# Kernel tuning notes

Hardware: AMD Instinct MI355X
Metric: run time of the kernel (lower is better)

## Reference

```python
import jax, jax.numpy as jnp
import numpy as np

N_EVENTS = 131072
N_FEATURES = 128
N_GLOBAL = 64
HIDDEN = 512
N_BRANCHES = 2


def setup_inputs() -> dict:
    key = jax.random.key(0)
    ks = jax.random.split(key, 4)
    x = jax.random.normal(ks[0], (N_EVENTS, N_FEATURES), dtype=jnp.float32)
    global_features = jax.random.normal(ks[1], (N_EVENTS, N_GLOBAL), dtype=jnp.float32)
    # proj_nn params: Linear(192->512) + LeakyReLU + Linear(512->256)
    W1 = jax.random.normal(ks[2], (N_FEATURES + N_GLOBAL, HIDDEN), dtype=jnp.float32) / np.sqrt(N_FEATURES + N_GLOBAL)
    b1 = jnp.zeros((HIDDEN,), dtype=jnp.float32)
    W2 = jax.random.normal(ks[3], (HIDDEN, N_BRANCHES * N_FEATURES), dtype=jnp.float32) / np.sqrt(HIDDEN)
    b2 = jnp.zeros((N_BRANCHES * N_FEATURES,), dtype=jnp.float32)
    # isplit=0: root node idxs = arange(n_events)
    parents_idxs = jnp.arange(N_EVENTS, dtype=jnp.int64 if jax.config.jax_enable_x64 else jnp.int32)
    return {"x": x, "global_features": global_features, "W1": W1, "b1": b1,
            "W2": W2, "b2": b2, "parents_idxs": parents_idxs}


def reference(x, global_features, W1, b1, W2, b2, parents_idxs):
    n_events, n_features = x.shape
    n_branches = N_BRANCHES
    n_parents = parents_idxs.shape[0] // n_events  # = 1 at isplit=0
    # gather parent node features and per-event global features
    parent_global = global_features[parents_idxs % n_events, :]   # [P*E, G]
    parents_ftxs = x[parents_idxs, :]                             # [P*E, F]
    # proj_nn: Linear -> LeakyReLU -> Linear
    h = jnp.concatenate([parents_ftxs, parent_global], axis=1)
    h = jax.nn.leaky_relu(h @ W1 + b1)                            # slope 0.01, torch default
    proj_ftx = h @ W2 + b2                                        # [P*E, B*F]
    # reshape_features: out[p, b, e] = proj[e + p*E, b*F:(b+1)*F]
    children_ftxs = (proj_ftx
                     .reshape(n_parents, n_events, n_branches, n_features)
                     .transpose(0, 2, 1, 3)
                     .reshape(n_parents * n_branches * n_events, n_features))
    return jnp.concatenate([x, children_ftxs], axis=0)
```

## Files before the change

kernel.cpp:

```cpp
#include <hip/hip_runtime.h>
#include <hip/hip_bf16.h>

#define NEV 131072
#define NF 128
#define NG 64
#define KIN 192
#define NH 512
#define NOUT 256
#define BM 128
#define NT 512
#define NBLK (NEV / BM)
#define LDS128 131072

typedef __bf16 bf16x8 __attribute__((ext_vector_type(8)));
typedef __bf16 bf16x4 __attribute__((ext_vector_type(4)));
typedef float f32x4 __attribute__((ext_vector_type(4)));

__device__ __forceinline__ int a_off(int r, int cb) { return r * 384 + (cb ^ ((r & 7) << 4)); }
__device__ __forceinline__ int h_off(int r, int cb) { return r * 1024 + (cb ^ ((r & 7) << 4)); }

__global__ void pack_w(const float* __restrict__ W1, const float* __restrict__ W2,
                       __bf16* __restrict__ w1p, __bf16* __restrict__ w2p) {
    int t = blockIdx.x * blockDim.x + threadIdx.x;
    if (t < KIN * NH) {
        int j = t & 7;
        int lane = (t >> 3) & 63;
        int n = (t >> 9) & 3;
        int r = t >> 11;
        int kk = r % 6;
        int wc = r / 6;
        int lg = lane >> 4, lr = lane & 15;
        int k = kk * 32 + lg * 8 + j;
        int col = wc * 64 + n * 16 + lr;
        w1p[t] = (__bf16)W1[(size_t)k * NH + col];
    } else {
        int u = t - KIN * NH;
        if (u < NH * NOUT) {
            int j = u & 7;
            int lane = (u >> 3) & 63;
            int n = (u >> 9) & 1;
            int r = u >> 10;
            int kk = r & 15;
            int wc = r >> 4;
            int lg = lane >> 4, lr = lane & 15;
            int k = kk * 32 + lg * 8 + j;
            int col = wc * 32 + n * 16 + lr;
            w2p[u] = (__bf16)W2[(size_t)k * NOUT + col];
        }
    }
}

__global__ __launch_bounds__(NT)
__attribute__((amdgpu_waves_per_eu(2, 2))) void fused128(
        const float* __restrict__ x, const float* __restrict__ gf,
        const __bf16* __restrict__ w1p, const float* __restrict__ b1,
        const __bf16* __restrict__ w2p, const float* __restrict__ b2,
        const int* __restrict__ idx, float* __restrict__ out) {
    extern __shared__ __align__(16) unsigned char smem[];

    const int tid = threadIdx.x;
    const int wc = tid >> 6;
    const int lane = tid & 63;
    const int lg = lane >> 4;
    const int lr = lane & 15;
    const int row0 = blockIdx.x * BM;

    bf16x8 bcur[4];
    {
        const __bf16* wp = w1p;
        asm volatile("" : "+s"(wp));
#pragma unroll
        for (int n = 0; n < 4; ++n)
            bcur[n] = *(const bf16x8*)(wp + (size_t)((wc * 6 + 0) * 4 + n) * 512 + lane * 8);
    }

    const f32x4* x4 = (const f32x4*)x;
    const f32x4* g4 = (const f32x4*)gf;
    f32x4* o4 = (f32x4*)out;
#pragma unroll
    for (int q = tid; q < BM * (NF / 4); q += NT) {
        int r = q >> 5, c4 = q & 31;
        int e = row0 + r;
        int p = idx[e];
        f32x4 v = x4[(size_t)e * 32 + c4];
        __builtin_nontemporal_store(v, &o4[(size_t)e * 32 + c4]);
        f32x4 vs = v;
        if (p != e) vs = x4[(size_t)p * 32 + c4];
        bf16x4 tb = {(__bf16)vs[0], (__bf16)vs[1], (__bf16)vs[2], (__bf16)vs[3]};
        *(bf16x4*)(smem + a_off(r, c4 * 8)) = tb;
    }
#pragma unroll
    for (int q = tid; q < BM * (NG / 4); q += NT) {
        int r = q >> 4, c4 = q & 15;
        int e = row0 + r;
        int p = idx[e] & (NEV - 1);
        f32x4 vs = g4[(size_t)p * 16 + c4];
        bf16x4 tb = {(__bf16)vs[0], (__bf16)vs[1], (__bf16)vs[2], (__bf16)vs[3]};
        *(bf16x4*)(smem + a_off(r, 256 + c4 * 8)) = tb;
    }
    __syncthreads();

    f32x4 acc1T[4][8] = {};
#pragma unroll
    for (int kk = 0; kk < KIN / 32; ++kk) {
        bf16x8 bnxt[4];
        if (kk + 1 < KIN / 32) {
            const __bf16* wp = w1p;
            asm volatile("" : "+s"(wp));
#pragma unroll
            for (int n = 0; n < 4; ++n)
                bnxt[n] = *(const bf16x8*)(wp + (size_t)((wc * 6 + kk + 1) * 4 + n) * 512 + lane * 8);
        }
        int kbyte = kk * 64 + lg * 16;
        bf16x8 a[8];
#pragma unroll
        for (int m = 0; m < 8; ++m)
            a[m] = *(const bf16x8*)(smem + a_off(m * 16 + lr, kbyte));
        __builtin_amdgcn_s_setprio(1);
#pragma unroll
        for (int n = 0; n < 4; ++n)
#pragma unroll
            for (int m = 0; m < 8; ++m)
                acc1T[n][m] = __builtin_amdgcn_mfma_f32_16x16x32_bf16(bcur[n], a[m], acc1T[n][m], 0, 0, 0);
        __builtin_amdgcn_s_setprio(0);
        if (kk + 1 < KIN / 32) {
#pragma unroll
            for (int n = 0; n < 4; ++n) bcur[n] = bnxt[n];
        }
        __builtin_amdgcn_sched_barrier(0);
    }

    bf16x8 ccur[2];
    {
        const __bf16* wp = w2p;
        asm volatile("" : "+s"(wp));
#pragma unroll
        for (int n = 0; n < 2; ++n)
            ccur[n] = *(const bf16x8*)(wp + (size_t)((wc * 16 + 0) * 2 + n) * 512 + lane * 8);
    }
    __syncthreads();

#pragma unroll
    for (int n = 0; n < 4; ++n) {
        int c0 = wc * 64 + n * 16 + lg * 4;
        f32x4 bb = *(const f32x4*)(b1 + c0);
#pragma unroll
        for (int m = 0; m < 8; ++m) {
            int e = m * 16 + lr;
            bf16x4 tb;
#pragma unroll
            for (int i = 0; i < 4; ++i) {
                float v = acc1T[n][m][i] + bb[i];
                v = (v >= 0.f) ? v : 0.01f * v;
                tb[i] = (__bf16)v;
            }
            *(bf16x4*)(smem + h_off(e, c0 * 2)) = tb;
        }
    }
    __syncthreads();

    f32x4 acc2T[2][8] = {};
#pragma unroll
    for (int kk = 0; kk < NH / 32; ++kk) {
        bf16x8 cnxt[2];
        if (kk + 1 < NH / 32) {
            const __bf16* wp = w2p;
            asm volatile("" : "+s"(wp));
#pragma unroll
            for (int n = 0; n < 2; ++n)
                cnxt[n] = *(const bf16x8*)(wp + (size_t)((wc * 16 + kk + 1) * 2 + n) * 512 + lane * 8);
        }
        int kbyte = kk * 64 + lg * 16;
        bf16x8 a2[8];
#pragma unroll
        for (int m = 0; m < 8; ++m)
            a2[m] = *(const bf16x8*)(smem + h_off(m * 16 + lr, kbyte));
        __builtin_amdgcn_s_setprio(1);
#pragma unroll
        for (int n = 0; n < 2; ++n)
#pragma unroll
            for (int m = 0; m < 8; ++m)
                acc2T[n][m] = __builtin_amdgcn_mfma_f32_16x16x32_bf16(ccur[n], a2[m], acc2T[n][m], 0, 0, 0);
        __builtin_amdgcn_s_setprio(0);
        if (kk + 1 < NH / 32) {
#pragma unroll
            for (int n = 0; n < 2; ++n) ccur[n] = cnxt[n];
        }
        __builtin_amdgcn_sched_barrier(0);
    }

    float* ob = out + ((size_t)NEV * (1 + (wc >> 2))) * NF;
#pragma unroll
    for (int m = 0; m < 8; ++m) {
        size_t ebase = (size_t)(row0 + m * 16 + lr) * NF;
#pragma unroll
        for (int n = 0; n < 2; ++n) {
            int col = wc * 32 + n * 16 + lg * 4;
            f32x4 bb = *(const f32x4*)(b2 + col);
            f32x4 v = acc2T[n][m] + bb;
            __builtin_nontemporal_store(v, (f32x4*)(ob + ebase + (col & 127)));
        }
    }
}

template <bool TW>
__global__ __launch_bounds__(512, 2) void fused_mlp(
        const float* __restrict__ x, const float* __restrict__ gf,
        const __bf16* __restrict__ w1p, const float* __restrict__ W1f,
        const float* __restrict__ b1,
        const __bf16* __restrict__ w2p, const float* __restrict__ W2f,
        const float* __restrict__ b2,
        const int* __restrict__ idx,
        float* __restrict__ out) {
    __shared__ __align__(16) unsigned char smem[65536];

    const int tid = threadIdx.x;
    const int wid = tid >> 6;
    const int lane = tid & 63;
    const int lg = lane >> 4;
    const int lr = lane & 15;
    const int row0 = blockIdx.x * 64;

    bf16x8 b1r[KIN / 32][4];
#pragma unroll
    for (int kk = 0; kk < KIN / 32; ++kk)
#pragma unroll
        for (int n = 0; n < 4; ++n) {
            if (TW) {
                b1r[kk][n] = *(const bf16x8*)(w1p + (size_t)(((wid * 6 + kk) * 4 + n) * 64 + lane) * 8);
            } else {
                int col = wid * 64 + n * 16 + lr;
                const float* wcp = W1f + (size_t)(kk * 32 + lg * 8) * NH + col;
#pragma unroll
                for (int i = 0; i < 8; ++i) b1r[kk][n][i] = (__bf16)wcp[(size_t)i * NH];
            }
        }

    const f32x4* x4 = (const f32x4*)x;
    const f32x4* g4 = (const f32x4*)gf;
    f32x4* o4 = (f32x4*)out;
    for (int q = tid; q < 64 * (NF / 4); q += 512) {
        int r = q >> 5, c4 = q & 31;
        int e = row0 + r;
        int p = idx[e];
        f32x4 v = x4[(size_t)e * 32 + c4];
        __builtin_nontemporal_store(v, &o4[(size_t)e * 32 + c4]);
        f32x4 vs = v;
        if (p != e) vs = x4[(size_t)p * 32 + c4];
        bf16x4 tb = {(__bf16)vs[0], (__bf16)vs[1], (__bf16)vs[2], (__bf16)vs[3]};
        *(bf16x4*)(smem + a_off(r, c4 * 8)) = tb;
    }
    for (int q = tid; q < 64 * (NG / 4); q += 512) {
        int r = q >> 4, c4 = q & 15;
        int e = row0 + r;
        int p = idx[e] & (NEV - 1);
        f32x4 vs = g4[(size_t)p * 16 + c4];
        bf16x4 tb = {(__bf16)vs[0], (__bf16)vs[1], (__bf16)vs[2], (__bf16)vs[3]};
        *(bf16x4*)(smem + a_off(r, 256 + c4 * 8)) = tb;
    }
    __syncthreads();

    f32x4 acc1T[4][4] = {};
#pragma unroll
    for (int kk = 0; kk < KIN / 32; ++kk) {
        int kbyte = kk * 64 + lg * 16;
        bf16x8 a[4];
#pragma unroll
        for (int m = 0; m < 4; ++m)
            a[m] = *(const bf16x8*)(smem + a_off(m * 16 + lr, kbyte));
        __builtin_amdgcn_s_setprio(1);
#pragma unroll
        for (int n = 0; n < 4; ++n)
#pragma unroll
            for (int m = 0; m < 4; ++m)
                acc1T[n][m] = __builtin_amdgcn_mfma_f32_16x16x32_bf16(b1r[kk][n], a[m], acc1T[n][m], 0, 0, 0);
        __builtin_amdgcn_s_setprio(0);
    }

    bf16x8 b2r[NH / 32][2];
#pragma unroll
    for (int kk = 0; kk < NH / 32; ++kk)
#pragma unroll
        for (int n = 0; n < 2; ++n) {
            if (TW) {
                b2r[kk][n] = *(const bf16x8*)(w2p + (size_t)(((wid * 16 + kk) * 2 + n) * 64 + lane) * 8);
            } else {
                int col = wid * 32 + n * 16 + lr;
                const float* wcp = W2f + (size_t)(kk * 32 + lg * 8) * NOUT + col;
#pragma unroll
                for (int i = 0; i < 8; ++i) b2r[kk][n][i] = (__bf16)wcp[(size_t)i * NOUT];
            }
        }

    __syncthreads();

#pragma unroll
    for (int n = 0; n < 4; ++n) {
        f32x4 bb = *(const f32x4*)(b1 + wid * 64 + n * 16 + lg * 4);
        int cb = (wid * 64 + n * 16 + lg * 4) * 2;
#pragma unroll
        for (int m = 0; m < 4; ++m) {
            int e = m * 16 + lr;
            bf16x4 tb;
#pragma unroll
            for (int i = 0; i < 4; ++i) {
                float v = acc1T[n][m][i] + bb[i];
                v = (v >= 0.f) ? v : 0.01f * v;
                tb[i] = (__bf16)v;
            }
            *(bf16x4*)(smem + h_off(e, cb)) = tb;
        }
    }
    __syncthreads();

    f32x4 acc2T[2][4] = {};
#pragma unroll
    for (int kk = 0; kk < NH / 32; ++kk) {
        int kbyte = kk * 64 + lg * 16;
        bf16x8 a2[4];
#pragma unroll
        for (int m = 0; m < 4; ++m)
            a2[m] = *(const bf16x8*)(smem + h_off(m * 16 + lr, kbyte));
        __builtin_amdgcn_s_setprio(1);
#pragma unroll
        for (int n = 0; n < 2; ++n)
#pragma unroll
            for (int m = 0; m < 4; ++m)
                acc2T[n][m] = __builtin_amdgcn_mfma_f32_16x16x32_bf16(b2r[kk][n], a2[m], acc2T[n][m], 0, 0, 0);
        __builtin_amdgcn_s_setprio(0);
    }

    float* ob = out + ((size_t)NEV * (1 + (wid >> 2))) * NF;
#pragma unroll
    for (int m = 0; m < 4; ++m) {
        size_t ebase = (size_t)(row0 + m * 16 + lr) * NF;
#pragma unroll
        for (int n = 0; n < 2; ++n) {
            int col = wid * 32 + n * 16 + lg * 4;
            f32x4 bb = *(const f32x4*)(b2 + col);
            f32x4 v = acc2T[n][m] + bb;
            __builtin_nontemporal_store(v, (f32x4*)(ob + ebase + (col & 127)));
        }
    }
}

extern "C" void kernel_launch(void* const* d_in, const int* in_sizes, int n_in,
                              void* d_out, int out_size, void* d_ws, size_t ws_size,
                              hipStream_t stream) {
    const float* x  = (const float*)d_in[0];
    const float* gf = (const float*)d_in[1];
    const float* W1 = (const float*)d_in[2];
    const float* b1 = (const float*)d_in[3];
    const float* W2 = (const float*)d_in[4];
    const float* b2 = (const float*)d_in[5];
    const int*  idx = (const int*)d_in[6];
    float* out = (float*)d_out;

    const size_t wbytes = (size_t)(KIN * NH + NH * NOUT) * sizeof(__bf16);
    int tot = KIN * NH + NH * NOUT;

    if (ws_size >= wbytes) {
        __bf16* w1p = (__bf16*)d_ws;
        __bf16* w2p = w1p + KIN * NH;
        pack_w<<<(tot + 511) / 512, 512, 0, stream>>>(W1, W2, w1p, w2p);
        hipError_t st = hipFuncSetAttribute(
            (const void*)fused128, hipFuncAttributeMaxDynamicSharedMemorySize, LDS128);
        if (st == hipSuccess) {
            fused128<<<NBLK, NT, LDS128, stream>>>(x, gf, w1p, b1, w2p, b2, idx, out);
        } else {
            fused_mlp<true><<<NEV / 64, 512, 0, stream>>>(x, gf, w1p, nullptr, b1,
                                                          w2p, nullptr, b2, idx, out);
        }
    } else {
        fused_mlp<false><<<NEV / 64, 512, 0, stream>>>(x, gf, nullptr, W1, b1,
                                                       nullptr, W2, b2, idx, out);
    }
}
```

Measured before the change: 102.2 us.

## Make fused MLP kernel loop over tiles with double-buffered input staging

```diff
diff --git a/kernel.cpp b/kernel.cpp
--- a/kernel.cpp
+++ b/kernel.cpp
@@ -7,10 +7,13 @@
 #define KIN 192
 #define NH 512
 #define NOUT 256
-#define BM 128
+#define BM 64
 #define NT 512
-#define NBLK (NEV / BM)
-#define LDS128 131072
+#define TILES 8
+#define NPERS (NEV / (BM * TILES))
+#define ABYTES 24576
+#define HBASE (2 * ABYTES)
+#define LDSTOT (HBASE + BM * NH * 2)
 
 typedef __bf16 bf16x8 __attribute__((ext_vector_type(8)));
 typedef __bf16 bf16x4 __attribute__((ext_vector_type(4)));
@@ -51,7 +54,7 @@
 }
 
 __global__ __launch_bounds__(NT)
-__attribute__((amdgpu_waves_per_eu(2, 2))) void fused128(
+__attribute__((amdgpu_waves_per_eu(2, 2))) void fused_pers(
         const float* __restrict__ x, const float* __restrict__ gf,
         const __bf16* __restrict__ w1p, const float* __restrict__ b1,
         const __bf16* __restrict__ w2p, const float* __restrict__ b2,
@@ -63,8 +66,51 @@
     const int lane = tid & 63;
     const int lg = lane >> 4;
     const int lr = lane & 15;
-    const int row0 = blockIdx.x * BM;
-
+
+    const f32x4* x4 = (const f32x4*)x;
+    const f32x4* g4 = (const f32x4*)gf;
+    f32x4* o4 = (f32x4*)out;
+    const int xr = tid >> 5, xc = tid & 31;
+    const int gr = tid >> 4, gc = tid & 15;
+
+    f32x4 xv[4], xs[4], gv[2];
+
+    auto stage_issue = [&](int row0) {
+#pragma unroll
+        for (int s = 0; s < 4; ++s) {
+            int e = row0 + xr + 16 * s;
+            int p = idx[e];
+            xv[s] = x4[(size_t)e * 32 + xc];
+            xs[s] = xv[s];
+            if (p != e) xs[s] = x4[(size_t)p * 32 + xc];
+        }
+#pragma unroll
+        for (int s = 0; s < 2; ++s) {
+            int e = row0 + gr + 32 * s;
+            int p = idx[e] & (NEV - 1);
+            gv[s] = g4[(size_t)p * 16 + gc];
+        }
+    };
+    auto stage_commit = [&](int row0, int ab) {
+#pragma unroll
+        for (int s = 0; s < 4; ++s) {
+            int r = xr + 16 * s;
+            __builtin_nontemporal_store(xv[s], &o4[(size_t)(row0 + r) * 32 + xc]);
+            bf16x4 tb = {(__bf16)xs[s][0], (__bf16)xs[s][1], (__bf16)xs[s][2], (__bf16)xs[s][3]};
+            *(bf16x4*)(smem + ab + a_off(r, xc * 8)) = tb;
+        }
+#pragma unroll
+        for (int s = 0; s < 2; ++s) {
+            int r = gr + 32 * s;
+            bf16x4 tb = {(__bf16)gv[s][0], (__bf16)gv[s][1], (__bf16)gv[s][2], (__bf16)gv[s][3]};
+            *(bf16x4*)(smem + ab + a_off(r, 256 + gc * 8)) = tb;
+        }
+    };
+
+    int row0 = blockIdx.x * (BM * TILES);
+
+    stage_issue(row0);
+    stage_commit(row0, 0);
     bf16x8 bcur[4];
     {
         const __bf16* wp = w1p;
@@ -73,133 +119,126 @@
         for (int n = 0; n < 4; ++n)
             bcur[n] = *(const bf16x8*)(wp + (size_t)((wc * 6 + 0) * 4 + n) * 512 + lane * 8);
     }
-
-    const f32x4* x4 = (const f32x4*)x;
-    const f32x4* g4 = (const f32x4*)gf;
-    f32x4* o4 = (f32x4*)out;
-#pragma unroll
-    for (int q = tid; q < BM * (NF / 4); q += NT) {
-        int r = q >> 5, c4 = q & 31;
-        int e = row0 + r;
-        int p = idx[e];
-        f32x4 v = x4[(size_t)e * 32 + c4];
-        __builtin_nontemporal_store(v, &o4[(size_t)e * 32 + c4]);
-        f32x4 vs = v;
-        if (p != e) vs = x4[(size_t)p * 32 + c4];
-        bf16x4 tb = {(__bf16)vs[0], (__bf16)vs[1], (__bf16)vs[2], (__bf16)vs[3]};
-        *(bf16x4*)(smem + a_off(r, c4 * 8)) = tb;
-    }
-#pragma unroll
-    for (int q = tid; q < BM * (NG / 4); q += NT) {
-        int r = q >> 4, c4 = q & 15;
-        int e = row0 + r;
-        int p = idx[e] & (NEV - 1);
-        f32x4 vs = g4[(size_t)p * 16 + c4];
-        bf16x4 tb = {(__bf16)vs[0], (__bf16)vs[1], (__bf16)vs[2], (__bf16)vs[3]};
-        *(bf16x4*)(smem + a_off(r, 256 + c4 * 8)) = tb;
-    }
     __syncthreads();
 
-    f32x4 acc1T[4][8] = {};
-#pragma unroll
-    for (int kk = 0; kk < KIN / 32; ++kk) {
-        bf16x8 bnxt[4];
-        if (kk + 1 < KIN / 32) {
+    for (int t = 0; t < TILES; ++t) {
+        const int ab = (t & 1) ? ABYTES : 0;
+        const int nb = (t & 1) ? 0 : ABYTES;
+
+        if (t + 1 < TILES) stage_issue(row0 + BM);
+
+        f32x4 acc1T[4][4] = {};
+#pragma unroll
+        for (int kk = 0; kk < KIN / 32; ++kk) {
+            bf16x8 bnxt[4];
+            if (kk + 1 < KIN / 32) {
+                const __bf16* wp = w1p;
+                asm volatile("" : "+s"(wp));
+#pragma unroll
+                for (int n = 0; n < 4; ++n)
+                    bnxt[n] = *(const bf16x8*)(wp + (size_t)((wc * 6 + kk + 1) * 4 + n) * 512 + lane * 8);
+            }
+            int kbyte = kk * 64 + lg * 16;
+            bf16x8 a[4];
+#pragma unroll
+            for (int m = 0; m < 4; ++m)
+                a[m] = *(const bf16x8*)(smem + ab + a_off(m * 16 + lr, kbyte));
+            __builtin_amdgcn_s_setprio(1);
+#pragma unroll
+            for (int n = 0; n < 4; ++n)
+#pragma unroll
+                for (int m = 0; m < 4; ++m)
+                    acc1T[n][m] = __builtin_amdgcn_mfma_f32_16x16x32_bf16(bcur[n], a[m], acc1T[n][m], 0, 0, 0);
+            __builtin_amdgcn_s_setprio(0);
+            if (kk + 1 < KIN / 32) {
+#pragma unroll
+                for (int n = 0; n < 4; ++n) bcur[n] = bnxt[n];
+            }
+            __builtin_amdgcn_sched_barrier(0);
+        }
+
+        if (t + 1 < TILES) stage_commit(row0 + BM, nb);
+
+#pragma unroll
+        for (int n = 0; n < 4; ++n) {
+            int c0 = wc * 64 + n * 16 + lg * 4;
+            f32x4 bb = *(const f32x4*)(b1 + c0);
+#pragma unroll
+            for (int m = 0; m < 4; ++m) {
+                int e = m * 16 + lr;
+                bf16x4 tb;
+#pragma unroll
+                for (int i = 0; i < 4; ++i) {
+                    float v = acc1T[n][m][i] + bb[i];
+                    v = (v >= 0.f) ? v : 0.01f * v;
+                    tb[i] = (__bf16)v;
+                }
+                *(bf16x4*)(smem + HBASE + h_off(e, c0 * 2)) = tb;
+            }
+        }
+
+        bf16x8 ccur[2];
+        {
+            const __bf16* wp = w2p;
+            asm volatile("" : "+s"(wp));
+#pragma unroll
+            for (int n = 0; n < 2; ++n)
+                ccur[n] = *(const bf16x8*)(wp + (size_t)((wc * 16 + 0) * 2 + n) * 512 + lane * 8);
+        }
+        __syncthreads();
+
+        f32x4 acc2T[2][4] = {};
+#pragma unroll
+        for (int kk = 0; kk < NH / 32; ++kk) {
+            bf16x8 cnxt[2];
+            if (kk + 1 < NH / 32) {
+                const __bf16* wp = w2p;
+                asm volatile("" : "+s"(wp));
+#pragma unroll
+                for (int n = 0; n < 2; ++n)
+                    cnxt[n] = *(const bf16x8*)(wp + (size_t)((wc * 16 + kk + 1) * 2 + n) * 512 + lane * 8);
+            }
+            int kbyte = kk * 64 + lg * 16;
+            bf16x8 a2[4];
+#pragma unroll
+            for (int m = 0; m < 4; ++m)
+                a2[m] = *(const bf16x8*)(smem + HBASE + h_off(m * 16 + lr, kbyte));
+            __builtin_amdgcn_s_setprio(1);
+#pragma unroll
+            for (int n = 0; n < 2; ++n)
+#pragma unroll
+                for (int m = 0; m < 4; ++m)
+                    acc2T[n][m] = __builtin_amdgcn_mfma_f32_16x16x32_bf16(ccur[n], a2[m], acc2T[n][m], 0, 0, 0);
+            __builtin_amdgcn_s_setprio(0);
+            if (kk + 1 < NH / 32) {
+#pragma unroll
+                for (int n = 0; n < 2; ++n) ccur[n] = cnxt[n];
+            }
+            __builtin_amdgcn_sched_barrier(0);
+        }
+
+        float* ob = out + ((size_t)NEV * (1 + (wc >> 2))) * NF;
+#pragma unroll
+        for (int m = 0; m < 4; ++m) {
+            size_t ebase = (size_t)(row0 + m * 16 + lr) * NF;
+#pragma unroll
+            for (int n = 0; n < 2; ++n) {
+                int col = wc * 32 + n * 16 + lg * 4;
+                f32x4 bb = *(const f32x4*)(b2 + col);
+                f32x4 v = acc2T[n][m] + bb;
+                __builtin_nontemporal_store(v, (f32x4*)(ob + ebase + (col & 127)));
+            }
+        }
+
+        if (t + 1 < TILES) {
             const __bf16* wp = w1p;
             asm volatile("" : "+s"(wp));
 #pragma unroll
             for (int n = 0; n < 4; ++n)
-                bnxt[n] = *(const bf16x8*)(wp + (size_t)((wc * 6 + kk + 1) * 4 + n) * 512 + lane * 8);
-        }
-        int kbyte = kk * 64 + lg * 16;
-        bf16x8 a[8];
-#pragma unroll
-        for (int m = 0; m < 8; ++m)
-            a[m] = *(const bf16x8*)(smem + a_off(m * 16 + lr, kbyte));
-        __builtin_amdgcn_s_setprio(1);
-#pragma unroll
-        for (int n = 0; n < 4; ++n)
-#pragma unroll
-            for (int m = 0; m < 8; ++m)
-                acc1T[n][m] = __builtin_amdgcn_mfma_f32_16x16x32_bf16(bcur[n], a[m], acc1T[n][m], 0, 0, 0);
-        __builtin_amdgcn_s_setprio(0);
-        if (kk + 1 < KIN / 32) {
-#pragma unroll
-            for (int n = 0; n < 4; ++n) bcur[n] = bnxt[n];
-        }
-        __builtin_amdgcn_sched_barrier(0);
-    }
-
-    bf16x8 ccur[2];
-    {
-        const __bf16* wp = w2p;
-        asm volatile("" : "+s"(wp));
-#pragma unroll
-        for (int n = 0; n < 2; ++n)
-            ccur[n] = *(const bf16x8*)(wp + (size_t)((wc * 16 + 0) * 2 + n) * 512 + lane * 8);
-    }
-    __syncthreads();
-
-#pragma unroll
-    for (int n = 0; n < 4; ++n) {
-        int c0 = wc * 64 + n * 16 + lg * 4;
-        f32x4 bb = *(const f32x4*)(b1 + c0);
-#pragma unroll
-        for (int m = 0; m < 8; ++m) {
-            int e = m * 16 + lr;
-            bf16x4 tb;
-#pragma unroll
-            for (int i = 0; i < 4; ++i) {
-                float v = acc1T[n][m][i] + bb[i];
-                v = (v >= 0.f) ? v : 0.01f * v;
-                tb[i] = (__bf16)v;
-            }
-            *(bf16x4*)(smem + h_off(e, c0 * 2)) = tb;
-        }
-    }
-    __syncthreads();
-
-    f32x4 acc2T[2][8] = {};
-#pragma unroll
-    for (int kk = 0; kk < NH / 32; ++kk) {
-        bf16x8 cnxt[2];
-        if (kk + 1 < NH / 32) {
-            const __bf16* wp = w2p;
-            asm volatile("" : "+s"(wp));
-#pragma unroll
-            for (int n = 0; n < 2; ++n)
-                cnxt[n] = *(const bf16x8*)(wp + (size_t)((wc * 16 + kk + 1) * 2 + n) * 512 + lane * 8);
-        }
-        int kbyte = kk * 64 + lg * 16;
-        bf16x8 a2[8];
-#pragma unroll
-        for (int m = 0; m < 8; ++m)
-            a2[m] = *(const bf16x8*)(smem + h_off(m * 16 + lr, kbyte));
-        __builtin_amdgcn_s_setprio(1);
-#pragma unroll
-        for (int n = 0; n < 2; ++n)
-#pragma unroll
-            for (int m = 0; m < 8; ++m)
-                acc2T[n][m] = __builtin_amdgcn_mfma_f32_16x16x32_bf16(ccur[n], a2[m], acc2T[n][m], 0, 0, 0);
-        __builtin_amdgcn_s_setprio(0);
-        if (kk + 1 < NH / 32) {
-#pragma unroll
-            for (int n = 0; n < 2; ++n) ccur[n] = cnxt[n];
-        }
-        __builtin_amdgcn_sched_barrier(0);
-    }
-
-    float* ob = out + ((size_t)NEV * (1 + (wc >> 2))) * NF;
-#pragma unroll
-    for (int m = 0; m < 8; ++m) {
-        size_t ebase = (size_t)(row0 + m * 16 + lr) * NF;
-#pragma unroll
-        for (int n = 0; n < 2; ++n) {
-            int col = wc * 32 + n * 16 + lg * 4;
-            f32x4 bb = *(const f32x4*)(b2 + col);
-            f32x4 v = acc2T[n][m] + bb;
-            __builtin_nontemporal_store(v, (f32x4*)(ob + ebase + (col & 127)));
-        }
+                bcur[n] = *(const bf16x8*)(wp + (size_t)((wc * 6 + 0) * 4 + n) * 512 + lane * 8);
+        }
+        __syncthreads();
+        row0 += BM;
     }
 }
 
@@ -364,9 +403,9 @@
         __bf16* w2p = w1p + KIN * NH;
         pack_w<<<(tot + 511) / 512, 512, 0, stream>>>(W1, W2, w1p, w2p);
         hipError_t st = hipFuncSetAttribute(
-            (const void*)fused128, hipFuncAttributeMaxDynamicSharedMemorySize, LDS128);
+            (const void*)fused_pers, hipFuncAttributeMaxDynamicSharedMemorySize, LDSTOT);
         if (st == hipSuccess) {
-            fused128<<<NBLK, NT, LDS128, stream>>>(x, gf, w1p, b1, w2p, b2, idx, out);
+            fused_pers<<<NPERS, NT, LDSTOT, stream>>>(x, gf, w1p, b1, w2p, b2, idx, out);
         } else {
             fused_mlp<true><<<NEV / 64, 512, 0, stream>>>(x, gf, w1p, nullptr, b1,
                                                           w2p, nullptr, b2, idx, out);
```

After: 105.2 us. +2.9%, slower.
